# Optimization experiments

Measured on AMD Instinct MI355X. Metric: run time of the kernel, lower is better.

Reference implementation:

```python
import jax, jax.numpy as jnp
import numpy as np

VOCAB = 8000
IN_FEATURES = 256
P = 8  # half-window; neighbor_num = 2*P
B, L = 16, 2048


def setup_inputs() -> dict:
    key = jax.random.key(0)
    k1, k2, k3, k4 = jax.random.split(key, 4)
    input_ids = jax.random.randint(k1, (B, L), 0, VOCAB, dtype=jnp.int32)
    # node_embedding: default torch init (normal), padding_idx=0 row zeroed
    node_emb = jax.random.normal(k2, (VOCAB, IN_FEATURES), dtype=jnp.float32)
    node_emb = node_emb.at[0].set(0.0)
    # edge_weight and node_weight re-initialized with xavier_uniform (padding row NOT re-zeroed, matching source)
    lim_e = float(np.sqrt(6.0 / (VOCAB * VOCAB + 1 + 1)))
    edge_w = jax.random.uniform(k3, (VOCAB * VOCAB + 1, 1), minval=-lim_e, maxval=lim_e, dtype=jnp.float32)
    lim_n = float(np.sqrt(6.0 / (VOCAB + 1)))
    node_w = jax.random.uniform(k4, (VOCAB, 1), minval=-lim_n, maxval=lim_n, dtype=jnp.float32)
    return {"input_ids": input_ids, "node_emb": node_emb, "edge_w": edge_w, "node_w": node_w}


def _neighbors(input_ids):
    # vectorized sliding-window neighbor construction (replaces the python loop)
    b, l = input_ids.shape
    xp = jnp.pad(input_ids, ((0, 0), (P, P)))  # (B, L+2P)
    offsets = jnp.concatenate([jnp.arange(P), jnp.arange(P + 1, 2 * P + 1)])  # (2P,)
    idx = jnp.arange(l)[:, None] + offsets[None, :]  # (L, 2P)
    NX = xp[:, idx]  # (B, L, 2P)
    EW = input_ids[:, :, None].astype(jnp.int32) * VOCAB + NX
    EW = jnp.where(NX == 0, 0, EW)
    return NX, EW


def reference(input_ids, node_emb, edge_w, node_w):
    NX, EW = _neighbors(input_ids)
    Ra = node_emb[NX]              # (B, L, 2P, D) gather
    Ean = edge_w[EW]               # (B, L, 2P, 1) gather
    Mn = jnp.max(Ra * Ean, axis=2)  # (B, L, D) max over neighbors
    Rn = node_emb[input_ids]       # (B, L, D)
    Nn = node_w[input_ids]         # (B, L, 1)
    y = (1.0 - Nn) * Mn + Nn * Rn   # gated sum
    return y.sum(axis=1)           # (B, D)
```

## Files before the change

### kernel.cpp

```cpp
#include <hip/hip_runtime.h>


#define VOCAB 8000
#define FDIM  256
#define PNB   8
#define NK    16
#define BB    16
#define LL    2048
#define CHUNK 16
#define WIN   (CHUNK + 2*PNB)
#define NCHUNK (LL / CHUNK)

__global__ __launch_bounds__(256) void gnn_kernel(
    const int*   __restrict__ ids,
    const float* __restrict__ emb,
    const float* __restrict__ edge_w,
    const float* __restrict__ node_w,
    float*       __restrict__ ws)
{
    __shared__ float s_emb[WIN][FDIM];
    __shared__ float s_ew [CHUNK][NK];
    __shared__ int   s_tok[WIN];
    __shared__ float s_nw [CHUNK];
    __shared__ float s_red[4][FDIM];

    const int b   = blockIdx.y;
    const int l0  = blockIdx.x * CHUNK;
    const int tid = threadIdx.x;
    const int* idrow = ids + b * LL;

    if (tid < WIN) {
        const int p = l0 - PNB + tid;
        int t = (p >= 0 && p < LL) ? idrow[p] : 0;
        t = (t < 0) ? 0 : ((t >= VOCAB) ? (VOCAB - 1) : t);
        s_tok[tid] = t;
    }
    __syncthreads();

    {
        const int ll = tid >> 4;
        const int k  = tid & (NK - 1);
        const int n  = s_tok[ll + k + (k >= PNB ? 1 : 0)];
        const int c  = s_tok[ll + PNB];
        const long long ei = (n == 0) ? 0LL : (long long)c * VOCAB + n;
        s_ew[ll][k] = __builtin_nontemporal_load(edge_w + ei);
        if (tid < CHUNK) s_nw[tid] = node_w[s_tok[tid + PNB]];
    }
    {
        #pragma unroll
        for (int j = 0; j < 8; ++j) {
            const int i    = tid + 256 * j;
            const int row  = i >> 6;
            const int col4 = (i & 63) << 2;
            const float4 v = *(const float4*)(emb + (size_t)s_tok[row] * FDIM + col4);
            *(float4*)&s_emb[row][col4] = v;
        }
    }
    __syncthreads();

    const int wave = tid >> 6;
    const int lane = tid & 63;
    const int f0   = lane << 2;
    const int base = wave << 2;

    float4 m[4], rc[4];
    #pragma unroll
    for (int q = 0; q < 4; ++q)
        m[q] = make_float4(-INFINITY, -INFINITY, -INFINITY, -INFINITY);

    #pragma unroll
    for (int j = 0; j < 20; ++j) {
        const float4 r = *(const float4*)&s_emb[base + j][f0];
        #pragma unroll
        for (int q = 0; q < 4; ++q) {
            const int d = j - q;
            if (d < 0 || d > 16) continue;
            if (d == 8) { rc[q] = r; continue; }
            const int   k = (d < 8) ? d : d - 1;
            const float e = s_ew[base + q][k];
            m[q].x = fmaxf(m[q].x, e * r.x);
            m[q].y = fmaxf(m[q].y, e * r.y);
            m[q].z = fmaxf(m[q].z, e * r.z);
            m[q].w = fmaxf(m[q].w, e * r.w);
        }
    }

    float4 acc = make_float4(0.f, 0.f, 0.f, 0.f);
    #pragma unroll
    for (int q = 0; q < 4; ++q) {
        const float nw = s_nw[base + q];
        const float w1 = 1.0f - nw;
        acc.x += w1 * m[q].x + nw * rc[q].x;
        acc.y += w1 * m[q].y + nw * rc[q].y;
        acc.z += w1 * m[q].z + nw * rc[q].z;
        acc.w += w1 * m[q].w + nw * rc[q].w;
    }

    ((float4*)s_red[wave])[lane] = acc;
    __syncthreads();

    const float s = s_red[0][tid] + s_red[1][tid] + s_red[2][tid] + s_red[3][tid];
    ws[((size_t)b * NCHUNK + blockIdx.x) * FDIM + tid] = s;
}

__global__ __launch_bounds__(256) void gnn_reduce(
    const float* __restrict__ ws,
    float*       __restrict__ out)
{
    const int b = blockIdx.x;
    const int f = threadIdx.x;
    const float* p = ws + (size_t)b * NCHUNK * FDIM + f;
    float s = 0.0f;
    #pragma unroll 8
    for (int c = 0; c < NCHUNK; ++c)
        s += p[(size_t)c * FDIM];
    out[b * FDIM + f] = s;
}

extern "C" void kernel_launch(void* const* d_in, const int* in_sizes, int n_in,
                              void* d_out, int out_size, void* d_ws, size_t ws_size,
                              hipStream_t stream) {
    const int*   ids    = nullptr;
    const float* emb    = nullptr;
    const float* edge_w = nullptr;
    const float* node_w = nullptr;
    for (int i = 0; i < n_in; ++i) {
        const long long sz = in_sizes[i];
        if      (sz == (long long)BB * LL)            ids    = (const int*)  d_in[i];
        else if (sz == (long long)VOCAB * FDIM)       emb    = (const float*)d_in[i];
        else if (sz == (long long)VOCAB * VOCAB + 1)  edge_w = (const float*)d_in[i];
        else if (sz == (long long)VOCAB)              node_w = (const float*)d_in[i];
    }
    float* out = (float*)d_out;
    float* ws  = (float*)d_ws;

    dim3 grid(NCHUNK, BB);
    gnn_kernel<<<grid, 256, 0, stream>>>(ids, emb, edge_w, node_w, ws);
    gnn_reduce<<<dim3(BB), 256, 0, stream>>>(ws, out);
}
```

Before: 318.2 us.

## Process two chunks per block with register-staged prefetch of next embedding window

Each block now handles two 16-token chunks. Both chunks' edge-weight gathers are issued up front, and the first window's embeddings are loaded into registers before being written to shared memory, so the loads overlap. The second chunk's embedding window is prefetched into registers after the first chunk's compute, then swapped into shared memory between barriers. This halves the grid and the partial-sum workspace and hides some gather latency, at the cost of more registers, extra syncs, and re-fetching the overlapping halo rows.

```diff
diff --git a/kernel.cpp b/kernel.cpp
--- a/kernel.cpp
+++ b/kernel.cpp
@@ -1,15 +1,18 @@
 #include <hip/hip_runtime.h>
 
 
-#define VOCAB 8000
-#define FDIM  256
-#define PNB   8
-#define NK    16
-#define BB    16
-#define LL    2048
-#define CHUNK 16
-#define WIN   (CHUNK + 2*PNB)
-#define NCHUNK (LL / CHUNK)
+#define VOCAB  8000
+#define FDIM   256
+#define PNB    8
+#define NK     16
+#define BB     16
+#define LL     2048
+#define CHUNK  16
+#define CPB    2
+#define SPAN   (CHUNK * CPB)
+#define WIN    (CHUNK + 2*PNB)
+#define TOKW   (SPAN + 2*PNB)
+#define NBLK   (LL / SPAN)
 
 __global__ __launch_bounds__(256) void gnn_kernel(
     const int*   __restrict__ ids,
@@ -19,17 +22,18 @@
     float*       __restrict__ ws)
 {
     __shared__ float s_emb[WIN][FDIM];
-    __shared__ float s_ew [CHUNK][NK];
-    __shared__ int   s_tok[WIN];
-    __shared__ float s_nw [CHUNK];
+    __shared__ float s_ew [CPB][CHUNK][NK];
+    __shared__ int   s_tok[TOKW];
+    __shared__ float s_nw [SPAN];
     __shared__ float s_red[4][FDIM];
 
     const int b   = blockIdx.y;
-    const int l0  = blockIdx.x * CHUNK;
+    const int bx  = blockIdx.x;
+    const int l0  = bx * SPAN;
     const int tid = threadIdx.x;
     const int* idrow = ids + b * LL;
 
-    if (tid < WIN) {
+    if (tid < TOKW) {
         const int p = l0 - PNB + tid;
         int t = (p >= 0 && p < LL) ? idrow[p] : 0;
         t = (t < 0) ? 0 : ((t >= VOCAB) ? (VOCAB - 1) : t);
@@ -37,24 +41,35 @@
     }
     __syncthreads();
 
-    {
-        const int ll = tid >> 4;
-        const int k  = tid & (NK - 1);
-        const int n  = s_tok[ll + k + (k >= PNB ? 1 : 0)];
-        const int c  = s_tok[ll + PNB];
-        const long long ei = (n == 0) ? 0LL : (long long)c * VOCAB + n;
-        s_ew[ll][k] = __builtin_nontemporal_load(edge_w + ei);
-        if (tid < CHUNK) s_nw[tid] = node_w[s_tok[tid + PNB]];
+    const int ll = tid >> 4;
+    const int k  = tid & (NK - 1);
+    const int ko = k + (k >= PNB ? 1 : 0);
+    const int n0 = s_tok[ll + ko];
+    const int c0 = s_tok[ll + PNB];
+    const int n1 = s_tok[CHUNK + ll + ko];
+    const int c1 = s_tok[CHUNK + ll + PNB];
+    const float e0 = __builtin_nontemporal_load(
+        edge_w + ((n0 == 0) ? 0LL : (long long)c0 * VOCAB + n0));
+    const float e1 = __builtin_nontemporal_load(
+        edge_w + ((n1 == 0) ? 0LL : (long long)c1 * VOCAB + n1));
+
+    float4 rr[8];
+    #pragma unroll
+    for (int j = 0; j < 8; ++j) {
+        const int i    = tid + 256 * j;
+        const int row  = i >> 6;
+        const int col4 = (i & 63) << 2;
+        rr[j] = *(const float4*)(emb + (size_t)s_tok[row] * FDIM + col4);
     }
-    {
-        #pragma unroll
-        for (int j = 0; j < 8; ++j) {
-            const int i    = tid + 256 * j;
-            const int row  = i >> 6;
-            const int col4 = (i & 63) << 2;
-            const float4 v = *(const float4*)(emb + (size_t)s_tok[row] * FDIM + col4);
-            *(float4*)&s_emb[row][col4] = v;
-        }
+    s_ew[0][ll][k] = e0;
+    s_ew[1][ll][k] = e1;
+    if (tid < SPAN) s_nw[tid] = node_w[s_tok[tid + PNB]];
+    #pragma unroll
+    for (int j = 0; j < 8; ++j) {
+        const int i    = tid + 256 * j;
+        const int row  = i >> 6;
+        const int col4 = (i & 63) << 2;
+        *(float4*)&s_emb[row][col4] = rr[j];
     }
     __syncthreads();
 
@@ -63,44 +78,67 @@
     const int f0   = lane << 2;
     const int base = wave << 2;
 
-    float4 m[4], rc[4];
-    #pragma unroll
-    for (int q = 0; q < 4; ++q)
-        m[q] = make_float4(-INFINITY, -INFINITY, -INFINITY, -INFINITY);
+    float4 acc = make_float4(0.f, 0.f, 0.f, 0.f);
 
-    #pragma unroll
-    for (int j = 0; j < 20; ++j) {
-        const float4 r = *(const float4*)&s_emb[base + j][f0];
+    #pragma unroll 1
+    for (int ch = 0; ch < CPB; ++ch) {
+        float4 m[4], rc[4];
+        #pragma unroll
+        for (int q = 0; q < 4; ++q)
+            m[q] = make_float4(-INFINITY, -INFINITY, -INFINITY, -INFINITY);
+
+        #pragma unroll
+        for (int j = 0; j < 20; ++j) {
+            const float4 r = *(const float4*)&s_emb[base + j][f0];
+            #pragma unroll
+            for (int q = 0; q < 4; ++q) {
+                const int d = j - q;
+                if (d < 0 || d > 16) continue;
+                if (d == 8) { rc[q] = r; continue; }
+                const int   kk = (d < 8) ? d : d - 1;
+                const float e  = s_ew[ch][base + q][kk];
+                m[q].x = fmaxf(m[q].x, e * r.x);
+                m[q].y = fmaxf(m[q].y, e * r.y);
+                m[q].z = fmaxf(m[q].z, e * r.z);
+                m[q].w = fmaxf(m[q].w, e * r.w);
+            }
+        }
         #pragma unroll
         for (int q = 0; q < 4; ++q) {
-            const int d = j - q;
-            if (d < 0 || d > 16) continue;
-            if (d == 8) { rc[q] = r; continue; }
-            const int   k = (d < 8) ? d : d - 1;
-            const float e = s_ew[base + q][k];
-            m[q].x = fmaxf(m[q].x, e * r.x);
-            m[q].y = fmaxf(m[q].y, e * r.y);
-            m[q].z = fmaxf(m[q].z, e * r.z);
-            m[q].w = fmaxf(m[q].w, e * r.w);
+            const float nw = s_nw[ch * CHUNK + base + q];
+            const float w1 = 1.0f - nw;
+            acc.x += w1 * m[q].x + nw * rc[q].x;
+            acc.y += w1 * m[q].y + nw * rc[q].y;
+            acc.z += w1 * m[q].z + nw * rc[q].z;
+            acc.w += w1 * m[q].w + nw * rc[q].w;
         }
-    }
 
-    float4 acc = make_float4(0.f, 0.f, 0.f, 0.f);
-    #pragma unroll
-    for (int q = 0; q < 4; ++q) {
-        const float nw = s_nw[base + q];
-        const float w1 = 1.0f - nw;
-        acc.x += w1 * m[q].x + nw * rc[q].x;
-        acc.y += w1 * m[q].y + nw * rc[q].y;
-        acc.z += w1 * m[q].z + nw * rc[q].z;
-        acc.w += w1 * m[q].w + nw * rc[q].w;
+        if (ch == 0) {
+            float4 r2[8];
+            #pragma unroll
+            for (int j = 0; j < 8; ++j) {
+                const int i    = tid + 256 * j;
+                const int row  = i >> 6;
+                const int col4 = (i & 63) << 2;
+                r2[j] = *(const float4*)(emb + (size_t)s_tok[CHUNK + row] * FDIM + col4);
+            }
+            __syncthreads();
+            #pragma unroll
+            for (int j = 0; j < 8; ++j) {
+                const int i    = tid + 256 * j;
+                const int row  = i >> 6;
+                const int col4 = (i & 63) << 2;
+                *(float4*)&s_emb[row][col4] = r2[j];
+            }
+            __syncthreads();
+        }
     }
 
     ((float4*)s_red[wave])[lane] = acc;
     __syncthreads();
 
     const float s = s_red[0][tid] + s_red[1][tid] + s_red[2][tid] + s_red[3][tid];
-    ws[((size_t)b * NCHUNK + blockIdx.x) * FDIM + tid] = s;
+    ws[((size_t)b * NBLK + bx) * FDIM + tid] = s;
 }
 
 __global__ __launch_bounds__(256) void gnn_reduce(
@@ -109,10 +147,10 @@
 {
     const int b = blockIdx.x;
     const int f = threadIdx.x;
-    const float* p = ws + (size_t)b * NCHUNK * FDIM + f;
+    const float* p = ws + (size_t)b * NBLK * FDIM + f;
     float s = 0.0f;
     #pragma unroll 8
-    for (int c = 0; c < NCHUNK; ++c)
+    for (int c = 0; c < NBLK; ++c)
         s += p[(size_t)c * FDIM];
     out[b * FDIM + f] = s;
 }
@@ -134,7 +172,7 @@
     float* out = (float*)d_out;
     float* ws  = (float*)d_ws;
 
-    dim3 grid(NCHUNK, BB);
+    dim3 grid(NBLK, BB);
     gnn_kernel<<<grid, 256, 0, stream>>>(ids, emb, edge_w, node_w, ws);
     gnn_reduce<<<dim3(BB), 256, 0, stream>>>(ws, out);
 }
```

New measurement: 327.1 us. +2.8%, slower.
